# Performance work log

Hardware: AMD Instinct MI355X
Metric: run time of the kernel (lower is better)

## Reference

```python
import math
import jax, jax.numpy as jnp
import numpy as np

RADIUS = 3
KSIZE = 2 * RADIUS + 1
TOP_K = 8
SINKHORN_ITERS = 5


def _avg_pool_nopad(x, k, r):
    """avg_pool2d over last two dims with count_include_pad=False. x: [..., H, W]."""
    nd = x.ndim
    win = (1,) * (nd - 2) + (k, k)
    strides = (1,) * nd
    pad = [(0, 0)] * (nd - 2) + [(r, r), (r, r)]
    s = jax.lax.reduce_window(x, jnp.array(0.0, x.dtype), jax.lax.add, win, strides, pad)
    ones = jnp.ones(x.shape[-2:], x.dtype)
    cnt = jax.lax.reduce_window(ones, jnp.array(0.0, x.dtype), jax.lax.add, (k, k), (1, 1), [(r, r), (r, r)])
    return s / cnt


def _geometric_scores(src_pos, cand_pos, H, W):
    """src_pos: [B,N,2], cand_pos: [B,N,K,2] -> [B,N,K]."""
    B, N, K, _ = cand_pos.shape
    src_2d = src_pos.reshape(B, H, W, 2).transpose(0, 3, 1, 2)            # [B,2,H,W]
    cand = cand_pos.transpose(0, 2, 1, 3).reshape(B, K, H, W, 2)
    cand = cand.transpose(0, 1, 4, 2, 3)                                   # [B,K,2,H,W]
    disp = cand - src_2d[:, None]                                          # [B,K,2,H,W]
    mean_disp = _avg_pool_nopad(disp, KSIZE, RADIUS)
    mean_sq = _avg_pool_nopad(disp ** 2, KSIZE, RADIUS)
    var = jnp.clip(mean_sq - mean_disp ** 2, 0.0, None)
    total_var = var.sum(axis=2).reshape(B, K, N)                           # [B,K,N]
    score = 1.0 / (1.0 + total_var * 100.0)
    return score.transpose(0, 2, 1)                                        # [B,N,K]


def _optimal_transport(scores, dustbin_score, iters):
    """scores: [B,M,N] -> log assignment [B,M,N] (SuperGlue-style Sinkhorn)."""
    scores = scores.astype(jnp.float32)
    B, M, N = scores.shape
    ds = dustbin_score.astype(jnp.float32)
    top = jnp.concatenate([scores, jnp.broadcast_to(ds, (B, M, 1))], axis=2)
    bot = jnp.concatenate([jnp.broadcast_to(ds, (B, 1, N)), jnp.zeros((B, 1, 1), jnp.float32)], axis=2)
    Z = jnp.concatenate([top, bot], axis=1)                                # [B,M+1,N+1]
    norm = -math.log(M + N)
    log_mu = jnp.full((M + 1,), norm, jnp.float32).at[M].set(math.log(N) + norm)
    log_nu = jnp.full((N + 1,), norm, jnp.float32).at[N].set(math.log(M) + norm)
    lse = jax.scipy.special.logsumexp

    def body(carry, _):
        u, v = carry
        u = log_mu - lse(Z + v[:, None, :], axis=2)
        v = log_nu - lse(Z + u[:, :, None], axis=1)
        return (u, v), None

    u0 = jnp.zeros((B, M + 1), jnp.float32)
    v0 = jnp.zeros((B, N + 1), jnp.float32)
    (u, v), _ = jax.lax.scan(body, (u0, v0), None, length=iters)
    log_assign = Z + u[:, :, None] + v[:, None, :]
    return log_assign[:, :M, :N]


def setup_inputs() -> dict:
    key = jax.random.key(0)
    ks = jax.random.split(key, 4)
    B, N, C, H, W = 2, 4096, 128, 64, 64
    return {
        "feat_A": jax.random.normal(ks[0], (B, N, C), jnp.float32),
        "feat_B": jax.random.normal(ks[1], (B, N, C), jnp.float32),
        "pos_A": jax.random.uniform(ks[2], (B, N, 2), jnp.float32),
        "pos_B": jax.random.uniform(ks[3], (B, N, 2), jnp.float32),
        "dustbin_score": jnp.float32(-1.0),
        "geo_weight": jnp.float32(0.5),
        "current_temp": jnp.float32(0.05),
        "H": H,
        "W": W,
    }


def reference(feat_A, feat_B, pos_A, pos_B, dustbin_score, geo_weight, current_temp, H, W):
    B, N, C = feat_A.shape
    eps = 1e-12  # torch F.normalize eps
    norm_A = feat_A / jnp.clip(jnp.linalg.norm(feat_A, axis=-1, keepdims=True), eps, None)
    norm_B = feat_B / jnp.clip(jnp.linalg.norm(feat_B, axis=-1, keepdims=True), eps, None)
    raw_sim = jnp.einsum('bmc,bnc->bmn', norm_A, norm_B)
    scores = raw_sim / current_temp

    log_assign = _optimal_transport(scores, dustbin_score, SINKHORN_ITERS).astype(scores.dtype)
    ot_prob = jnp.exp(log_assign)                                          # [B,N,N]
    prob_dist = ot_prob / (ot_prob.sum(axis=-1, keepdims=True) + 1e-08)
    base_expected = jnp.einsum('bmn,bnd->bmd', prob_dist, pos_B)           # [B,N,2]

    topk_values, topk_idx = jax.lax.top_k(ot_prob, TOP_K)                  # [B,N,K]
    gather_pos = jax.vmap(lambda p, i: p[i])                               # p:[N,2], i:[N,K]
    topk_positions = gather_pos(pos_B, topk_idx)                           # [B,N,K,2]

    geo_scores = _geometric_scores(pos_A, topk_positions, H, W)            # [B,N,K]
    gw = jnp.clip(geo_weight, 0.0, 2.0)
    combined = topk_values + gw * geo_scores
    soft_w = jax.nn.softmax(combined / current_temp, axis=-1)
    refined_pos = (topk_positions * soft_w[..., None]).sum(axis=2)         # [B,N,2]
    offset = refined_pos - jax.lax.stop_gradient(base_expected)
    refined_warp = base_expected + offset

    entropy = -(prob_dist * jnp.log(prob_dist + 1e-08)).sum(axis=-1)       # [B,N]
    return refined_warp, entropy, raw_sim, geo_scores
```

## Files before the change

kernel.cpp:

```cpp
#include <hip/hip_runtime.h>
#include <math.h>

#define BB 2
#define NN 4096
#define CC 128
#define TK 8
#define USTR 4104

#define NORM_C  (-9.010913347279288f)
#define DUST_C  (-0.6931471805599453f)

__device__ __forceinline__ float block_sum4(float s, int t, float* sb){
  #pragma unroll
  for (int off = 32; off > 0; off >>= 1) s += __shfl_xor(s, off);
  if ((t & 63) == 0) sb[t >> 6] = s;
  __syncthreads();
  return sb[0] + sb[1] + sb[2] + sb[3];
}

extern "C" __global__ __launch_bounds__(256)
void k_norm(const float* __restrict__ fA, const float* __restrict__ fB,
            float* __restrict__ nA, float* __restrict__ nB){
  int gw   = (blockIdx.x * 256 + threadIdx.x) >> 6;
  int lane = threadIdx.x & 63;
  const float* src; float* dst;
  if (gw < BB*NN){ src = fA + (size_t)gw*CC; dst = nA + (size_t)gw*CC; }
  else { int r = gw - BB*NN; src = fB + (size_t)r*CC; dst = nB + (size_t)r*CC; }
  float2 x = ((const float2*)src)[lane];
  float ss = x.x*x.x + x.y*x.y;
  #pragma unroll
  for (int off = 32; off > 0; off >>= 1) ss += __shfl_xor(ss, off);
  float inv = 1.0f / fmaxf(sqrtf(ss), 1e-12f);
  ((float2*)dst)[lane] = make_float2(x.x*inv, x.y*inv);
}

extern "C" __global__ __launch_bounds__(256)
void k_gemm(const float* __restrict__ nA, const float* __restrict__ nB, float* __restrict__ sim){
  __shared__ float sA[32][132];
  __shared__ float sB[32][132];
  const int t  = threadIdx.x;
  const int b  = blockIdx.z;
  const int m0 = blockIdx.y << 7, n0 = blockIdx.x << 7;
  const float* Ab = nA + ((size_t)b*NN + m0)*CC;
  const float* Bb = nB + ((size_t)b*NN + n0)*CC;
  const int tx = t & 15, ty = t >> 4;
  float acc[8][8];
  #pragma unroll
  for (int i = 0; i < 8; i++)
    #pragma unroll
    for (int j = 0; j < 8; j++) acc[i][j] = 0.f;

  #pragma unroll 1
  for (int kc = 0; kc < 4; kc++){
    if (kc) __syncthreads();
    #pragma unroll
    for (int i = 0; i < 4; i++){
      int fi = t + (i << 8);
      int r  = fi >> 3, c4 = fi & 7;
      float4 av = *(const float4*)(Ab + (size_t)r*CC + (kc<<5) + (c4<<2));
      float4 bv = *(const float4*)(Bb + (size_t)r*CC + (kc<<5) + (c4<<2));
      int kk = c4 << 2;
      sA[kk+0][r]=av.x; sA[kk+1][r]=av.y; sA[kk+2][r]=av.z; sA[kk+3][r]=av.w;
      sB[kk+0][r]=bv.x; sB[kk+1][r]=bv.y; sB[kk+2][r]=bv.z; sB[kk+3][r]=bv.w;
    }
    __syncthreads();
    #pragma unroll 4
    for (int k = 0; k < 32; k++){
      float4 a0 = *(const float4*)&sA[k][ty<<2];
      float4 a1 = *(const float4*)&sA[k][64 + (ty<<2)];
      float4 b0 = *(const float4*)&sB[k][tx<<2];
      float4 b1 = *(const float4*)&sB[k][64 + (tx<<2)];
      float av[8] = {a0.x,a0.y,a0.z,a0.w,a1.x,a1.y,a1.z,a1.w};
      float bw[8] = {b0.x,b0.y,b0.z,b0.w,b1.x,b1.y,b1.z,b1.w};
      #pragma unroll
      for (int i = 0; i < 8; i++)
        #pragma unroll
        for (int j = 0; j < 8; j++)
          acc[i][j] = fmaf(av[i], bw[j], acc[i][j]);
    }
  }
  float* Cb = sim + ((size_t)b*NN + m0)*NN + n0;
  #pragma unroll
  for (int i = 0; i < 8; i++){
    int mr = (i < 4) ? ((ty<<2) + i) : (64 + (ty<<2) + (i-4));
    float* cp = Cb + (size_t)mr*NN;
    *(float4*)(cp + (tx<<2))      = make_float4(acc[i][0],acc[i][1],acc[i][2],acc[i][3]);
    *(float4*)(cp + 64 + (tx<<2)) = make_float4(acc[i][4],acc[i][5],acc[i][6],acc[i][7]);
  }
}

extern "C" __global__ __launch_bounds__(256)
void k_u(const float* __restrict__ sim, const float* __restrict__ v, float* __restrict__ u,
         const float* __restrict__ dsp, const float* __restrict__ tpp){
  int row = blockIdx.x, b = blockIdx.y, t = threadIdx.x;
  float invt = 1.0f / tpp[0], ds = dsp[0];
  const float4* vb4 = (const float4*)(v + b*USTR);
  float s0 = 0.f, s1 = 0.f, s2 = 0.f, s3 = 0.f;
  if (row < NN){
    const float4* sr4 = (const float4*)(sim + ((size_t)b*NN + row)*NN);
    #pragma unroll
    for (int i = 0; i < 4; i++){
      int q = t + (i<<8);
      float4 sv = sr4[q]; float4 vv = vb4[q];
      s0 += __expf(fmaf(sv.x, invt, vv.x));
      s1 += __expf(fmaf(sv.y, invt, vv.y));
      s2 += __expf(fmaf(sv.z, invt, vv.z));
      s3 += __expf(fmaf(sv.w, invt, vv.w));
    }
  } else {
    #pragma unroll
    for (int i = 0; i < 4; i++){
      int q = t + (i<<8);
      float4 vv = vb4[q];
      s0 += __expf(ds + vv.x);
      s1 += __expf(ds + vv.y);
      s2 += __expf(ds + vv.z);
      s3 += __expf(ds + vv.w);
    }
  }
  float s = (s0 + s1) + (s2 + s3);
  if (t == 0) s += __expf((row < NN ? ds : 0.0f) + v[b*USTR + NN]);
  __shared__ float sb[4];
  float S = block_sum4(s, t, sb);
  if (t == 0) u[b*USTR + row] = (row < NN ? NORM_C : DUST_C) - __logf(S);
}

extern "C" __global__ __launch_bounds__(256)
void k_vA(const float* __restrict__ sim, const float* __restrict__ u,
          float* __restrict__ psum, const float* __restrict__ tpp){
  int t = threadIdx.x;
  int c4 = blockIdx.x*256 + t;
  int chunk = blockIdx.y, b = blockIdx.z;
  float invt = 1.0f / tpp[0];
  __shared__ float su[64];
  if (t < 64) su[t] = u[b*USTR + (chunk<<6) + t];
  __syncthreads();
  const float4* sp = (const float4*)(sim + ((size_t)b*NN + (chunk<<6))*NN) + c4;
  float ax = 0.f, ay = 0.f, az = 0.f, aw = 0.f;
  #pragma unroll 8
  for (int r = 0; r < 64; r++){
    float4 sv = sp[(size_t)r*(NN/4)];
    float uu = su[r];
    ax += __expf(fmaf(sv.x, invt, uu));
    ay += __expf(fmaf(sv.y, invt, uu));
    az += __expf(fmaf(sv.z, invt, uu));
    aw += __expf(fmaf(sv.w, invt, uu));
  }
  ((float4*)(psum + ((size_t)(b*64 + chunk))*NN))[c4] = make_float4(ax, ay, az, aw);
}

extern "C" __global__ __launch_bounds__(256)
void k_vB(const float* __restrict__ psum, const float* __restrict__ u,
          float* __restrict__ v, const float* __restrict__ dsp){
  int t = threadIdx.x, b = blockIdx.z;
  float ds = dsp[0];
  if (blockIdx.x < 16){
    int n = blockIdx.x*256 + t;
    float s = 0.f;
    #pragma unroll 16
    for (int c = 0; c < 64; c++) s += psum[((size_t)(b*64 + c))*NN + n];
    s += __expf(ds + u[b*USTR + NN]);
    v[b*USTR + n] = NORM_C - __logf(s);
  } else {
    float s0 = 0.f;
    #pragma unroll
    for (int i = 0; i < 16; i++){ int m = t + (i<<8); s0 += __expf(ds + u[b*USTR + m]); }
    if (t == 0) s0 += __expf(u[b*USTR + NN]);
    __shared__ float sb[4];
    float S = block_sum4(s0, t, sb);
    if (t == 0) v[b*USTR + NN] = DUST_C - __logf(S);
  }
}

extern "C" __global__ __launch_bounds__(256)
void k_final(const float* __restrict__ sim, const float* __restrict__ u, const float* __restrict__ v,
             const float* __restrict__ posB, float* __restrict__ entO,
             float* __restrict__ tval, int* __restrict__ tidx, float* __restrict__ tpos,
             float* __restrict__ bexp, const float* __restrict__ tpp){
  int m = blockIdx.x, b = blockIdx.y, t = threadIdx.x;
  float invt = 1.0f / tpp[0];
  const float4* sr4 = (const float4*)(sim + ((size_t)b*NN + m)*NN);
  const float4* vb4 = (const float4*)(v + b*USTR);
  float um = u[b*USTR + m];
  float p[16];
  float s_loc = 0.f;
  #pragma unroll
  for (int i = 0; i < 4; i++){
    int q = t + (i<<8);
    float4 sv = sr4[q]; float4 vv = vb4[q];
    p[4*i+0] = __expf(fmaf(sv.x, invt, um + vv.x));
    p[4*i+1] = __expf(fmaf(sv.y, invt, um + vv.y));
    p[4*i+2] = __expf(fmaf(sv.z, invt, um + vv.z));
    p[4*i+3] = __expf(fmaf(sv.w, invt, um + vv.w));
    s_loc += (p[4*i+0] + p[4*i+1]) + (p[4*i+2] + p[4*i+3]);
  }
  __shared__ float rs[4];
  float Sp = block_sum4(s_loc, t, rs) + 1e-8f;

  const float4* pb4 = (const float4*)(posB + (size_t)b*NN*2);
  float e = 0.f, bx = 0.f, by = 0.f;
  #pragma unroll
  for (int i = 0; i < 4; i++){
    int q = t + (i<<8);
    float4 q01 = pb4[2*q];
    float4 q23 = pb4[2*q + 1];
    float pd0 = p[4*i+0] / Sp, pd1 = p[4*i+1] / Sp;
    float pd2 = p[4*i+2] / Sp, pd3 = p[4*i+3] / Sp;
    e -= pd0 * __logf(pd0 + 1e-8f) + pd1 * __logf(pd1 + 1e-8f)
       + pd2 * __logf(pd2 + 1e-8f) + pd3 * __logf(pd3 + 1e-8f);
    bx = fmaf(pd0, q01.x, bx); by = fmaf(pd0, q01.y, by);
    bx = fmaf(pd1, q01.z, bx); by = fmaf(pd1, q01.w, by);
    bx = fmaf(pd2, q23.x, bx); by = fmaf(pd2, q23.y, by);
    bx = fmaf(pd3, q23.z, bx); by = fmaf(pd3, q23.w, by);
  }
  #pragma unroll
  for (int off = 32; off > 0; off >>= 1){
    e  += __shfl_xor(e, off);
    bx += __shfl_xor(bx, off);
    by += __shfl_xor(by, off);
  }
  __shared__ float re[4], rbx[4], rby[4];
  if ((t & 63) == 0){ re[t>>6] = e; rbx[t>>6] = bx; rby[t>>6] = by; }
  __syncthreads();
  if (t == 0){
    entO[(size_t)b*NN + m] = re[0]+re[1]+re[2]+re[3];
    bexp[((size_t)b*NN + m)*2 + 0] = rbx[0]+rbx[1]+rbx[2]+rbx[3];
    bexp[((size_t)b*NN + m)*2 + 1] = rby[0]+rby[1]+rby[2]+rby[3];
  }

  __shared__ float wv[4]; __shared__ int wi[4];
  size_t obase = ((size_t)b*NN + m)*TK;
  for (int r = 0; r < TK; r++){
    float bv = -INFINITY; int bi = 0x7fffffff;
    #pragma unroll
    for (int j = 0; j < 16; j++){
      int n = ((t + ((j>>2)<<8)) << 2) + (j & 3);
      if (p[j] > bv){ bv = p[j]; bi = n; }
    }
    #pragma unroll
    for (int off = 32; off > 0; off >>= 1){
      float ov = __shfl_xor(bv, off); int oi = __shfl_xor(bi, off);
      if (ov > bv || (ov == bv && oi < bi)){ bv = ov; bi = oi; }
    }
    if ((t & 63) == 0){ wv[t>>6] = bv; wi[t>>6] = bi; }
    __syncthreads();
    float Wv = wv[0]; int Wi = wi[0];
    #pragma unroll
    for (int i = 1; i < 4; i++){ if (wv[i] > Wv || (wv[i] == Wv && wi[i] < Wi)){ Wv = wv[i]; Wi = wi[i]; } }
    if (t == ((Wi >> 2) & 255)){
      int sl = ((Wi >> 10) << 2) | (Wi & 3);
      #pragma unroll
      for (int j = 0; j < 16; j++) if (j == sl) p[j] = -INFINITY;
    }
    if (t == 0){
      tval[obase + r] = Wv; tidx[obase + r] = Wi;
      tpos[(obase + r)*2 + 0] = posB[((size_t)b*NN + Wi)*2 + 0];
      tpos[(obase + r)*2 + 1] = posB[((size_t)b*NN + Wi)*2 + 1];
    }
    __syncthreads();
  }
}

extern "C" __global__ __launch_bounds__(1024)
void k_geo(const float* __restrict__ posA, const float* __restrict__ tpos,
           float* __restrict__ geoO){
  int k = blockIdx.x, b = blockIdx.y, t = threadIdx.x;
  __shared__ float dx[4096], dy[4096];
  #pragma unroll
  for (int i = 0; i < 4; i++){
    int px = t + (i<<10);
    float2 c = *(const float2*)(tpos + (((size_t)b*NN + px)*TK + k)*2);
    float2 s = *(const float2*)(posA + ((size_t)b*NN + px)*2);
    dx[px] = c.x - s.x; dy[px] = c.y - s.y;
  }
  __syncthreads();
  #pragma unroll
  for (int i = 0; i < 4; i++){
    int px = t + (i<<10);
    int h = px >> 6, w = px & 63;
    int h0 = max(h-3, 0), h1 = min(h+3, 63);
    int w0 = max(w-3, 0), w1 = min(w+3, 63);
    float sx = 0.f, sxx = 0.f, sy = 0.f, syy = 0.f;
    for (int hh = h0; hh <= h1; hh++){
      int ro = hh << 6;
      for (int ww = w0; ww <= w1; ww++){
        float a = dx[ro + ww]; sx += a; sxx = fmaf(a, a, sxx);
        float c2 = dy[ro + ww]; sy += c2; syy = fmaf(c2, c2, syy);
      }
    }
    float rc = 1.0f / (float)((h1-h0+1)*(w1-w0+1));
    float mxm = sx*rc, mym = sy*rc;
    float vx = fmaxf(sxx*rc - mxm*mxm, 0.f);
    float vy = fmaxf(syy*rc - mym*mym, 0.f);
    float tv = vx + vy;
    geoO[((size_t)b*NN + px)*TK + k] = 1.0f / (1.0f + tv*100.0f);
  }
}

extern "C" __global__ __launch_bounds__(256)
void k_refine(const float* __restrict__ tval, const float* __restrict__ tpos,
              const float* __restrict__ geo, const float* __restrict__ bexp,
              float* __restrict__ warpO, const float* __restrict__ gwp,
              const float* __restrict__ tpp){
  int id = blockIdx.x*256 + threadIdx.x;
  float gw = fminf(fmaxf(gwp[0], 0.f), 2.f);
  float invt = 1.0f / tpp[0];
  size_t base = (size_t)id * TK;
  float c[8], px[8], py[8];
  float cm = -INFINITY;
  #pragma unroll
  for (int k = 0; k < 8; k++){
    c[k]  = tval[base + k] + gw * geo[base + k];
    px[k] = tpos[(base + k)*2 + 0]; py[k] = tpos[(base + k)*2 + 1];
    cm = fmaxf(cm, c[k]);
  }
  float Ws = 0.f, rx = 0.f, ry = 0.f;
  #pragma unroll
  for (int k = 0; k < 8; k++){
    float w = expf((c[k] - cm)*invt);
    Ws += w; rx = fmaf(w, px[k], rx); ry = fmaf(w, py[k], ry);
  }
  rx /= Ws; ry /= Ws;
  float bxv = bexp[id*2 + 0], byv = bexp[id*2 + 1];
  warpO[id*2 + 0] = bxv + (rx - bxv);
  warpO[id*2 + 1] = byv + (ry - byv);
}

extern "C" void kernel_launch(void* const* d_in, const int* in_sizes, int n_in,
                              void* d_out, int out_size, void* d_ws, size_t ws_size,
                              hipStream_t stream){
  (void)in_sizes; (void)n_in; (void)out_size; (void)ws_size;
  const float* fA   = (const float*)d_in[0];
  const float* fB   = (const float*)d_in[1];
  const float* posA = (const float*)d_in[2];
  const float* posB = (const float*)d_in[3];
  const float* dsp  = (const float*)d_in[4];
  const float* gwp  = (const float*)d_in[5];
  const float* tpp  = (const float*)d_in[6];

  float* out   = (float*)d_out;
  float* warpO = out;
  float* entO  = out + (size_t)BB*NN*2;
  float* sim   = out + (size_t)BB*NN*2 + (size_t)BB*NN;
  float* geoO  = sim + (size_t)BB*NN*NN;

  float* u    = (float*)d_ws;
  float* v    = u + BB*USTR;
  float* psum = v + BB*USTR;
  float* tval = psum + (size_t)BB*64*NN;
  int*   tidx = (int*)(tval + BB*NN*TK);
  float* tpos = (float*)(tidx + BB*NN*TK);
  float* bexp = tpos + (size_t)BB*NN*TK*2;
  float* nA   = bexp + BB*NN*2;
  float* nB   = nA + (size_t)BB*NN*CC;

  hipMemsetAsync(u, 0, sizeof(float)*(size_t)BB*USTR*2, stream);

  k_norm<<<dim3(4096), dim3(256), 0, stream>>>(fA, fB, nA, nB);
  k_gemm<<<dim3(NN/128, NN/128, BB), dim3(256), 0, stream>>>(nA, nB, sim);

  for (int it = 0; it < 5; ++it){
    k_u <<<dim3(NN+1, BB), dim3(256), 0, stream>>>(sim, v, u, dsp, tpp);
    k_vA<<<dim3(4, 64, BB), dim3(256), 0, stream>>>(sim, u, psum, tpp);
    k_vB<<<dim3(17, 1, BB), dim3(256), 0, stream>>>(psum, u, v, dsp);
  }

  k_final<<<dim3(NN, BB), dim3(256), 0, stream>>>(sim, u, v, posB, entO,
                                                  tval, tidx, tpos, bexp, tpp);
  k_geo<<<dim3(TK, BB), dim3(1024), 0, stream>>>(posA, tpos, geoO);
  k_refine<<<dim3((BB*NN)/256), dim3(256), 0, stream>>>(tval, tpos, geoO, bexp,
                                                        warpO, gwp, tpp);
}
```

Measured before the change: 572.4 us.

## Fuse Sinkhorn row and column updates into one pass over the similarity matrix

Merges the u update and the column partial sums into a single kernel, so each Sinkhorn iteration reads the 2x4096x4096 similarity matrix once instead of twice. It reuses exp(sim/t + v) computed for the row normalisation and rescales it by the new u, with v removed later in the finish kernel via exp(-v_old). It also ping-pongs the v buffers and widens the partial-sum array to 256 parts. The costs are a larger psum reduction, LDS atomics, heavy register use (two float4[16] arrays) and possible precision loss from the exp(-v) rescale.

```diff
diff --git a/kernel.cpp b/kernel.cpp
--- a/kernel.cpp
+++ b/kernel.cpp
@@ -6,9 +6,11 @@
 #define CC 128
 #define TK 8
 #define USTR 4104
+#define PARTS 256
 
 #define NORM_C  (-9.010913347279288f)
 #define DUST_C  (-0.6931471805599453f)
+#define E_NORM  (1.220703125e-4f)
 
 __device__ __forceinline__ float block_sum4(float s, int t, float* sb){
   #pragma unroll
@@ -89,86 +91,111 @@
   }
 }
 
+extern "C" __global__ __launch_bounds__(256, 2)
+void k_uv(const float* __restrict__ sim, const float* __restrict__ v_in,
+          float* __restrict__ u, float* __restrict__ psum,
+          const float* __restrict__ dsp, const float* __restrict__ tpp){
+  const int b = blockIdx.y, blk = blockIdx.x, t = threadIdx.x;
+  const int wave = t >> 6, lane = t & 63;
+  const float invt = 1.0f / tpp[0], ds = dsp[0];
+  __shared__ float vcache[NN];
+  __shared__ float ctab[NN];
+  __shared__ float sb[4];
+  const float4* vin4 = (const float4*)(v_in + b*USTR);
+  #pragma unroll
+  for (int i = 0; i < 4; i++){
+    ((float4*)vcache)[t + (i<<8)] = vin4[t + (i<<8)];
+    ((float4*)ctab)[t + (i<<8)]   = make_float4(0.f,0.f,0.f,0.f);
+  }
+  __syncthreads();
+  const float vN = v_in[b*USTR + NN];
+
+  if (blk == PARTS){
+    float s = 0.f;
+    #pragma unroll
+    for (int i = 0; i < 16; i++) s += __expf(ds + vcache[t + (i<<8)]);
+    float S = block_sum4(s, t, sb);
+    if (t == 0) u[b*USTR + NN] = DUST_C - __logf(S + __expf(vN));
+    return;
+  }
+
+  const float4* vc4 = (const float4*)vcache;
+  float4 acc[16];
+  #pragma unroll
+  for (int j = 0; j < 16; j++) acc[j] = make_float4(0.f,0.f,0.f,0.f);
+
+  const int row0 = (blk << 4) + (wave << 2);
+  #pragma unroll 2
+  for (int r = 0; r < 4; r++){
+    const int row = row0 + r;
+    const float4* sr4 = (const float4*)(sim + ((size_t)b*NN + row)*NN);
+    float4 pv[16];
+    #pragma unroll
+    for (int j = 0; j < 16; j++) pv[j] = sr4[(j<<6) + lane];
+    float s = 0.f;
+    #pragma unroll
+    for (int j = 0; j < 16; j++){
+      float4 vv = vc4[(j<<6) + lane];
+      pv[j].x = __expf(fmaf(pv[j].x, invt, vv.x));
+      pv[j].y = __expf(fmaf(pv[j].y, invt, vv.y));
+      pv[j].z = __expf(fmaf(pv[j].z, invt, vv.z));
+      pv[j].w = __expf(fmaf(pv[j].w, invt, vv.w));
+      s += (pv[j].x + pv[j].y) + (pv[j].z + pv[j].w);
+    }
+    #pragma unroll
+    for (int off = 32; off > 0; off >>= 1) s += __shfl_xor(s, off);
+    s += __expf(ds + vN);
+    if (lane == 0) u[b*USTR + row] = NORM_C - __logf(s);
+    float w = E_NORM / s;
+    #pragma unroll
+    for (int j = 0; j < 16; j++){
+      acc[j].x = fmaf(pv[j].x, w, acc[j].x);
+      acc[j].y = fmaf(pv[j].y, w, acc[j].y);
+      acc[j].z = fmaf(pv[j].z, w, acc[j].z);
+      acc[j].w = fmaf(pv[j].w, w, acc[j].w);
+    }
+  }
+  #pragma unroll
+  for (int j = 0; j < 16; j++){
+    int base = (j<<8) + (lane<<2);
+    atomicAdd(&ctab[base+0], acc[j].x);
+    atomicAdd(&ctab[base+1], acc[j].y);
+    atomicAdd(&ctab[base+2], acc[j].z);
+    atomicAdd(&ctab[base+3], acc[j].w);
+  }
+  __syncthreads();
+  float4* po = (float4*)(psum + ((size_t)(b*PARTS + blk))*NN);
+  #pragma unroll
+  for (int i = 0; i < 4; i++) po[t + (i<<8)] = ((const float4*)ctab)[t + (i<<8)];
+}
+
 extern "C" __global__ __launch_bounds__(256)
-void k_u(const float* __restrict__ sim, const float* __restrict__ v, float* __restrict__ u,
-         const float* __restrict__ dsp, const float* __restrict__ tpp){
-  int row = blockIdx.x, b = blockIdx.y, t = threadIdx.x;
-  float invt = 1.0f / tpp[0], ds = dsp[0];
-  const float4* vb4 = (const float4*)(v + b*USTR);
-  float s0 = 0.f, s1 = 0.f, s2 = 0.f, s3 = 0.f;
-  if (row < NN){
-    const float4* sr4 = (const float4*)(sim + ((size_t)b*NN + row)*NN);
-    #pragma unroll
-    for (int i = 0; i < 4; i++){
-      int q = t + (i<<8);
-      float4 sv = sr4[q]; float4 vv = vb4[q];
-      s0 += __expf(fmaf(sv.x, invt, vv.x));
-      s1 += __expf(fmaf(sv.y, invt, vv.y));
-      s2 += __expf(fmaf(sv.z, invt, vv.z));
-      s3 += __expf(fmaf(sv.w, invt, vv.w));
-    }
-  } else {
-    #pragma unroll
-    for (int i = 0; i < 4; i++){
-      int q = t + (i<<8);
-      float4 vv = vb4[q];
-      s0 += __expf(ds + vv.x);
-      s1 += __expf(ds + vv.y);
-      s2 += __expf(ds + vv.z);
-      s3 += __expf(ds + vv.w);
-    }
-  }
-  float s = (s0 + s1) + (s2 + s3);
-  if (t == 0) s += __expf((row < NN ? ds : 0.0f) + v[b*USTR + NN]);
-  __shared__ float sb[4];
-  float S = block_sum4(s, t, sb);
-  if (t == 0) u[b*USTR + row] = (row < NN ? NORM_C : DUST_C) - __logf(S);
-}
-
-extern "C" __global__ __launch_bounds__(256)
-void k_vA(const float* __restrict__ sim, const float* __restrict__ u,
-          float* __restrict__ psum, const float* __restrict__ tpp){
-  int t = threadIdx.x;
-  int c4 = blockIdx.x*256 + t;
-  int chunk = blockIdx.y, b = blockIdx.z;
-  float invt = 1.0f / tpp[0];
-  __shared__ float su[64];
-  if (t < 64) su[t] = u[b*USTR + (chunk<<6) + t];
-  __syncthreads();
-  const float4* sp = (const float4*)(sim + ((size_t)b*NN + (chunk<<6))*NN) + c4;
-  float ax = 0.f, ay = 0.f, az = 0.f, aw = 0.f;
-  #pragma unroll 8
-  for (int r = 0; r < 64; r++){
-    float4 sv = sp[(size_t)r*(NN/4)];
-    float uu = su[r];
-    ax += __expf(fmaf(sv.x, invt, uu));
-    ay += __expf(fmaf(sv.y, invt, uu));
-    az += __expf(fmaf(sv.z, invt, uu));
-    aw += __expf(fmaf(sv.w, invt, uu));
-  }
-  ((float4*)(psum + ((size_t)(b*64 + chunk))*NN))[c4] = make_float4(ax, ay, az, aw);
-}
-
-extern "C" __global__ __launch_bounds__(256)
-void k_vB(const float* __restrict__ psum, const float* __restrict__ u,
-          float* __restrict__ v, const float* __restrict__ dsp){
-  int t = threadIdx.x, b = blockIdx.z;
-  float ds = dsp[0];
+void k_vfin(const float* __restrict__ psum, const float* __restrict__ u,
+            const float* __restrict__ v_in, float* __restrict__ v_out,
+            const float* __restrict__ dsp){
+  const int t = threadIdx.x, b = blockIdx.y;
+  const float ds = dsp[0];
   if (blockIdx.x < 16){
     int n = blockIdx.x*256 + t;
+    const float* pp = psum + (size_t)b*PARTS*NN + n;
+    float s0=0.f, s1=0.f, s2=0.f, s3=0.f;
+    #pragma unroll 4
+    for (int c = 0; c < PARTS; c += 4){
+      s0 += pp[(size_t)(c+0)*NN];
+      s1 += pp[(size_t)(c+1)*NN];
+      s2 += pp[(size_t)(c+2)*NN];
+      s3 += pp[(size_t)(c+3)*NN];
+    }
+    float colsum = ((s0+s1)+(s2+s3)) * __expf(-v_in[b*USTR + n]);
+    colsum += __expf(ds + u[b*USTR + NN]);
+    v_out[b*USTR + n] = NORM_C - __logf(colsum);
+  } else {
     float s = 0.f;
-    #pragma unroll 16
-    for (int c = 0; c < 64; c++) s += psum[((size_t)(b*64 + c))*NN + n];
-    s += __expf(ds + u[b*USTR + NN]);
-    v[b*USTR + n] = NORM_C - __logf(s);
-  } else {
-    float s0 = 0.f;
-    #pragma unroll
-    for (int i = 0; i < 16; i++){ int m = t + (i<<8); s0 += __expf(ds + u[b*USTR + m]); }
-    if (t == 0) s0 += __expf(u[b*USTR + NN]);
+    #pragma unroll
+    for (int i = 0; i < 16; i++){ int m = t + (i<<8); s += __expf(ds + u[b*USTR + m]); }
     __shared__ float sb[4];
-    float S = block_sum4(s0, t, sb);
-    if (t == 0) v[b*USTR + NN] = DUST_C - __logf(S);
+    float S = block_sum4(s, t, sb);
+    if (t == 0) v_out[b*USTR + NN] = DUST_C - __logf(S + __expf(u[b*USTR + NN]));
   }
 }
 
@@ -345,27 +372,29 @@
   float* geoO  = sim + (size_t)BB*NN*NN;
 
   float* u    = (float*)d_ws;
-  float* v    = u + BB*USTR;
-  float* psum = v + BB*USTR;
-  float* tval = psum + (size_t)BB*64*NN;
+  float* v_a  = u + BB*USTR;
+  float* v_b  = v_a + BB*USTR;
+  float* psum = v_b + BB*USTR;
+  float* tval = psum + (size_t)BB*PARTS*NN;
   int*   tidx = (int*)(tval + BB*NN*TK);
   float* tpos = (float*)(tidx + BB*NN*TK);
   float* bexp = tpos + (size_t)BB*NN*TK*2;
   float* nA   = bexp + BB*NN*2;
   float* nB   = nA + (size_t)BB*NN*CC;
 
-  hipMemsetAsync(u, 0, sizeof(float)*(size_t)BB*USTR*2, stream);
+  hipMemsetAsync(u, 0, sizeof(float)*(size_t)BB*USTR*3, stream);
 
   k_norm<<<dim3(4096), dim3(256), 0, stream>>>(fA, fB, nA, nB);
   k_gemm<<<dim3(NN/128, NN/128, BB), dim3(256), 0, stream>>>(nA, nB, sim);
 
+  float* vp = v_a; float* vn = v_b;
   for (int it = 0; it < 5; ++it){
-    k_u <<<dim3(NN+1, BB), dim3(256), 0, stream>>>(sim, v, u, dsp, tpp);
-    k_vA<<<dim3(4, 64, BB), dim3(256), 0, stream>>>(sim, u, psum, tpp);
-    k_vB<<<dim3(17, 1, BB), dim3(256), 0, stream>>>(psum, u, v, dsp);
-  }
-
-  k_final<<<dim3(NN, BB), dim3(256), 0, stream>>>(sim, u, v, posB, entO,
+    k_uv  <<<dim3(PARTS+1, BB), dim3(256), 0, stream>>>(sim, vp, u, psum, dsp, tpp);
+    k_vfin<<<dim3(17, BB), dim3(256), 0, stream>>>(psum, u, vp, vn, dsp);
+    float* tmp = vp; vp = vn; vn = tmp;
+  }
+
+  k_final<<<dim3(NN, BB), dim3(256), 0, stream>>>(sim, u, vp, posB, entO,
                                                   tval, tidx, tpos, bexp, tpp);
   k_geo<<<dim3(TK, BB), dim3(1024), 0, stream>>>(posA, tpos, geoO);
   k_refine<<<dim3((BB*NN)/256), dim3(256), 0, stream>>>(tval, tpos, geoO, bexp,
```

Result: slower. 835.9 us (+46.0%).
